# Kernel tuning notes

Measured on AMD Instinct MI355X. Metric: run time of the kernel, lower is better.

Reference implementation:

```python
import jax, jax.numpy as jnp
import numpy as np

N, E, NG = 4096, 8192, 256
AF, BF, H, L = 9, 4, 128, 3
LN_EPS = 1e-5


def _layernorm(x, g, b):
    mu = jnp.mean(x, axis=-1, keepdims=True)
    var = jnp.var(x, axis=-1, keepdims=True)
    return (x - mu) * jax.lax.rsqrt(var + LN_EPS) * g + b


def setup_inputs() -> dict:
    key = jax.random.key(0)
    ks = jax.random.split(key, 20)
    x = jax.random.normal(ks[0], (N, AF), dtype=jnp.float32)
    edge_index = jax.random.randint(ks[1], (2, E), 0, N, dtype=jnp.int64)
    edge_attr = jax.random.normal(ks[2], (E, BF), dtype=jnp.float32)
    batch = jnp.sort(jax.random.randint(ks[3], (N,), 0, NG, dtype=jnp.int64))
    s = lambda f: 1.0 / np.sqrt(f)
    return {
        "x": x, "edge_index": edge_index, "edge_attr": edge_attr, "batch": batch,
        "atom_w": jax.random.normal(ks[4], (AF, H), jnp.float32) * s(AF),
        "atom_b": jnp.zeros((H,), jnp.float32),
        # per-layer edge-network params, stacked over L layers
        "e1_w": jax.random.normal(ks[5], (L, BF, H), jnp.float32) * s(BF),
        "e1_b": jnp.zeros((L, H), jnp.float32),
        "e2_w": jax.random.normal(ks[6], (L, H, H * H), jnp.float32) * s(H),
        "e2_b": jnp.zeros((L, H * H), jnp.float32),
        "root_w": jax.random.normal(ks[7], (L, H, H), jnp.float32) * s(H),
        "conv_b": jnp.zeros((L, H), jnp.float32),
        "ln_g": jnp.ones((L, H), jnp.float32),
        "ln_b": jnp.zeros((L, H), jnp.float32),
        "head_w1": jax.random.normal(ks[8], (H, H // 2), jnp.float32) * s(H),
        "head_b1": jnp.zeros((H // 2,), jnp.float32),
        "head_w2": jax.random.normal(ks[9], (H // 2, 1), jnp.float32) * s(H // 2),
        "head_b2": jnp.zeros((1,), jnp.float32),
    }


def reference(x, edge_index, edge_attr, batch, atom_w, atom_b, e1_w, e1_b,
              e2_w, e2_b, root_w, conv_b, ln_g, ln_b, head_w1, head_b1,
              head_w2, head_b2):
    src, dst = edge_index[0], edge_index[1]
    h = jax.nn.relu(x @ atom_w + atom_b)  # [N, H]
    # in-degree for mean aggregation (empty -> 0 via clamp on denominator)
    deg = jax.ops.segment_sum(jnp.ones((E,), h.dtype), dst, num_segments=N)
    denom = jnp.maximum(deg, 1.0)[:, None]
    for l in range(L):
        # edge network: bond features -> per-edge HxH weight matrix
        eh = jax.nn.gelu(edge_attr @ e1_w[l] + e1_b[l], approximate=False)
        w = (eh @ e2_w[l] + e2_b[l]).reshape(E, H, H)  # [E, H, H]
        # gather source node features, per-edge matvec, scatter-mean to dst
        msg = jnp.einsum('ei,eio->eo', h[src], w)  # [E, H]
        agg = jax.ops.segment_sum(msg, dst, num_segments=N) / denom
        h_new = jax.nn.relu(agg + h @ root_w[l] + conv_b[l])
        h = _layernorm(h + h_new, ln_g[l], ln_b[l])
        # dropout: eval mode (identity)
    # global mean pool over graphs
    cnt = jnp.maximum(jax.ops.segment_sum(jnp.ones((N,), h.dtype), batch, num_segments=NG), 1.0)
    mol = jax.ops.segment_sum(h, batch, num_segments=NG) / cnt[:, None]
    hid = jax.nn.gelu(mol @ head_w1 + head_b1, approximate=False)
    logits = (hid @ head_w2 + head_b2).squeeze(-1)  # [NG]
    return logits
```

## Files before the change

kernel.cpp:

```cpp
#include <hip/hip_runtime.h>
#include <hip/hip_bf16.h>

#define N_NODES 4096
#define N_EDGES 8192
#define NGRAPH  256
#define AFEAT   9
#define BFEAT   4
#define H       128
#define NL      3
#define KS      129
#define SPLITS  8
#define SLICE_SH    16384
#define SLICE_BYTES 32768
#define HALF_BYTES  16384

typedef short short8 __attribute__((ext_vector_type(8)));
typedef short short4v __attribute__((ext_vector_type(4)));
typedef float f32x4 __attribute__((ext_vector_type(4)));

__device__ __forceinline__ short f2b(float f){
    union { float f; unsigned u; } c; c.f = f;
    unsigned r = c.u + 0x7FFFu + ((c.u >> 16) & 1u);
    return (short)(r >> 16);
}
__device__ __forceinline__ float b2f(short b){
    union { unsigned u; float f; } c;
    c.u = ((unsigned)(unsigned short)b) << 16;
    return c.f;
}
__device__ __forceinline__ float gelu_exact(float x){
    return 0.5f * x * (1.0f + erff(x * 0.70710678118654752440f));
}
__device__ __forceinline__ void async_copy16(const void* g, void* l){
    typedef __attribute__((address_space(1))) const char AS1C;
    typedef __attribute__((address_space(3))) char AS3;
    __builtin_amdgcn_global_load_lds((AS1C*)g, (AS3*)l, 16, 0, 0);
}

__global__ void k_prep_b(const float* __restrict__ e2w, const float* __restrict__ e2b,
                         short* __restrict__ bt){
    __shared__ float ts[H][33];
    int b  = blockIdx.x;
    int o0 = (b & 3) * 32;
    int k  = (b >> 2) % KS;
    int l  = (b >> 2) / KS;
    const float* src = (k < H) ? (e2w + ((size_t)l * H + k) * (H * H))
                               : (e2b + (size_t)l * (H * H));
    for (int idx = threadIdx.x; idx < H * 32; idx += 256){
        int i = idx >> 5, op = idx & 31;
        ts[i][op] = src[i * H + o0 + op];
    }
    __syncthreads();
    short* dst = bt + (size_t)(l * KS + k) * SLICE_SH;
    for (int idx = threadIdx.x; idx < 32 * H; idx += 256){
        int j    = idx & 7;
        int quad = (idx >> 3) & 3;
        int op   = (idx >> 5) & 31;
        int ic   = idx >> 10;
        int i    = ic * 32 + quad * 8 + j;
        int o    = o0 + op;
        dst[((((o >> 4) * 4 + ic) * 64) + quad * 16 + (o & 15)) * 8 + j] = f2b(ts[i][op]);
    }
}

__global__ void k_atom(const float* __restrict__ x, const float* __restrict__ aw,
                       const float* __restrict__ ab, float* __restrict__ h,
                       short* __restrict__ hb){
    __shared__ float xs[AFEAT];
    int n = blockIdx.x, o = threadIdx.x;
    if (o < AFEAT) xs[o] = x[n * AFEAT + o];
    __syncthreads();
    float a = ab[o];
    #pragma unroll
    for (int f = 0; f < AFEAT; ++f) a += xs[f] * aw[f * H + o];
    a = fmaxf(a, 0.0f);
    h[(size_t)n * H + o]  = a;
    hb[(size_t)n * H + o] = f2b(a);
}

__global__ void k_deg(const int* __restrict__ ei, int* __restrict__ ideg){
    int e = blockIdx.x * 256 + threadIdx.x;
    if (e < N_EDGES) atomicAdd(&ideg[ei[N_EDGES + e]], 1);
}

__global__ void k_scan(const int* __restrict__ ideg, int* __restrict__ row_ptr,
                       int* __restrict__ cursor){
    __shared__ int part[256];
    int t = threadIdx.x;
    int base = t * 16;
    int loc[16]; int s = 0;
    #pragma unroll
    for (int i = 0; i < 16; ++i){ loc[i] = s; s += ideg[base + i]; }
    part[t] = s;
    __syncthreads();
    if (t == 0){
        int run = 0;
        for (int i = 0; i < 256; ++i){ int v = part[i]; part[i] = run; run += v; }
        row_ptr[N_NODES] = run;
    }
    __syncthreads();
    int off = part[t];
    #pragma unroll
    for (int i = 0; i < 16; ++i){
        row_ptr[base + i] = off + loc[i];
        cursor[base + i]  = off + loc[i];
    }
}

__global__ void k_fill(const int* __restrict__ ei, int* __restrict__ cursor,
                       int* __restrict__ eidx){
    int e = blockIdx.x * 256 + threadIdx.x;
    if (e < N_EDGES){
        int d = ei[N_EDGES + e];
        int pos = atomicAdd(&cursor[d], 1);
        eidx[pos] = e;
    }
}

__global__ void k_edge_mlp(const float* __restrict__ ea, const float* __restrict__ w1,
                           const float* __restrict__ b1, short* __restrict__ ehT){
    __shared__ float as[BFEAT];
    int e = blockIdx.x, o = threadIdx.x;
    if (o < BFEAT) as[o] = ea[e * BFEAT + o];
    __syncthreads();
    #pragma unroll
    for (int l = 0; l < NL; ++l){
        float v = b1[l * H + o];
        #pragma unroll
        for (int f = 0; f < BFEAT; ++f) v += as[f] * w1[(l * BFEAT + f) * H + o];
        v = gelu_exact(v);
        ehT[((size_t)l * KS + o) * N_EDGES + e] = f2b(v);
        if (o == 0) ehT[((size_t)l * KS + H) * N_EDGES + e] = f2b(1.0f);
    }
}

__global__ __launch_bounds__(256, 2)
void k_msg_gemm(const short* __restrict__ bt, const short* __restrict__ ehT,
                const short* __restrict__ hb, const int* __restrict__ ei,
                float* __restrict__ parts, int l){
    __shared__ __align__(16) char smem[2 * HALF_BYTES + 17 * H * 2];
    short* ehs = (short*)(smem + 2 * HALF_BYTES);

    const int tid  = threadIdx.x;
    const int lane = tid & 63, w = tid >> 6;
    const int col  = lane & 15, quad = lane >> 4;
    const int wrow = w >> 1, wcol = w & 1;

    const int split = blockIdx.x & 7;
    const int oh    = (blockIdx.x >> 3) & 1;
    const int tile  = blockIdx.x >> 4;
    const int kbeg  = (KS * split) >> 3;
    const int kend  = (KS * (split + 1)) >> 3;
    const int kcnt  = kend - kbeg;
    const int ebase = tile * 128;

    for (int idx = tid; idx < kcnt * 128; idx += 256){
        int kk = idx >> 7, e = idx & 127;
        ehs[idx] = ehT[((size_t)(l * KS + kbeg + kk)) * N_EDGES + ebase + e];
    }

    short8 gf[4][4];
    #pragma unroll
    for (int m = 0; m < 4; ++m){
        int e = ebase + wrow * 64 + m * 16 + col;
        int s = ei[e];
        const char* gb = (const char*)hb + ((size_t)s * H + quad * 8) * 2;
        #pragma unroll
        for (int ic = 0; ic < 4; ++ic)
            gf[m][ic] = *(const short8*)(gb + ic * 64);
    }

    float acc[4][2][4];
    #pragma unroll
    for (int m = 0; m < 4; ++m)
        #pragma unroll
        for (int ot = 0; ot < 2; ++ot)
            #pragma unroll
            for (int r = 0; r < 4; ++r) acc[m][ot][r] = 0.0f;

    const char* bsrc = (const char*)bt + (size_t)(l * KS + kbeg) * SLICE_BYTES
                     + oh * HALF_BYTES;

    #pragma unroll
    for (int i = 0; i < 4; ++i){
        int c = w * 4 + i;
        async_copy16(bsrc + c * 1024 + lane * 16, smem + c * 1024 + lane * 16);
    }
    __syncthreads();

    for (int kk = 0; kk < kcnt; ++kk){
        __builtin_amdgcn_s_barrier();
        if (kk + 1 < kcnt){
            const char* g = bsrc + (size_t)(kk + 1) * SLICE_BYTES;
            char* d = smem + ((kk + 1) & 1) * HALF_BYTES;
            #pragma unroll
            for (int i = 0; i < 4; ++i){
                int c = w * 4 + i;
                async_copy16(g + c * 1024 + lane * 16, d + c * 1024 + lane * 16);
            }
            asm volatile("s_waitcnt vmcnt(4)" ::: "memory");
        } else {
            asm volatile("s_waitcnt vmcnt(0)" ::: "memory");
        }
        __builtin_amdgcn_s_barrier();

        const char* Bl = smem + (kk & 1) * HALF_BYTES;

        short4v ev[4];
        #pragma unroll
        for (int m = 0; m < 4; ++m)
            ev[m] = *(const short4v*)(ehs + kk * 128 + wrow * 64 + m * 16 + quad * 4);

        __builtin_amdgcn_s_setprio(1);
        #pragma unroll
        for (int ot = 0; ot < 2; ++ot){
            int tl = wcol * 2 + ot;
            short8 bf[4];
            #pragma unroll
            for (int ic = 0; ic < 4; ++ic)
                bf[ic] = *(const short8*)(Bl + (tl * 4 + ic) * 1024 + lane * 16);
            #pragma unroll
            for (int m = 0; m < 4; ++m){
                f32x4 U = {0.0f, 0.0f, 0.0f, 0.0f};
                #pragma unroll
                for (int ic = 0; ic < 4; ++ic)
                    U = __builtin_amdgcn_mfma_f32_16x16x32_bf16(gf[m][ic], bf[ic], U, 0, 0, 0);
                #pragma unroll
                for (int r = 0; r < 4; ++r)
                    acc[m][ot][r] += b2f(ev[m][r]) * U[r];
            }
        }
        __builtin_amdgcn_s_setprio(0);
    }

    float* pb = parts + (size_t)split * N_EDGES * H + (size_t)(ebase + wrow * 64) * H
              + oh * 64 + wcol * 32;
    #pragma unroll
    for (int m = 0; m < 4; ++m)
        #pragma unroll
        for (int r = 0; r < 4; ++r){
            float* row = pb + (m * 16 + quad * 4 + r) * H;
            #pragma unroll
            for (int ot = 0; ot < 2; ++ot)
                row[ot * 16 + col] = acc[m][ot][r];
        }
}

__global__ void k_node(const float* __restrict__ parts, const int* __restrict__ eidx,
                       const int* __restrict__ row_ptr,
                       const float* __restrict__ rw, const float* __restrict__ cb,
                       const float* __restrict__ lg, const float* __restrict__ lb,
                       float* __restrict__ h, short* __restrict__ hb, int l){
    __shared__ float hs[H];
    __shared__ float rsum[2], rsq[2];
    int n = blockIdx.x, o = threadIdx.x;
    float hv = h[(size_t)n * H + o];
    hs[o] = hv;
    int p0 = row_ptr[n], p1 = row_ptr[n + 1];
    float a = 0.0f;
    for (int p = p0; p < p1; ++p){
        const float* pr = parts + (size_t)eidx[p] * H + o;
        #pragma unroll
        for (int s = 0; s < SPLITS; ++s) a += pr[(size_t)s * N_EDGES * H];
    }
    int d = p1 - p0;
    a *= 1.0f / (float)(d > 0 ? d : 1);
    __syncthreads();
    float root = cb[l * H + o];
    const float* W = rw + (size_t)l * H * H;
    #pragma unroll 8
    for (int i = 0; i < H; ++i) root += hs[i] * W[i * H + o];
    float hn = fmaxf(a + root, 0.0f);
    float v  = hv + hn;
    float s = v, q = v * v;
    #pragma unroll
    for (int off = 32; off > 0; off >>= 1){
        s += __shfl_down(s, off, 64);
        q += __shfl_down(q, off, 64);
    }
    if ((o & 63) == 0){ rsum[o >> 6] = s; rsq[o >> 6] = q; }
    __syncthreads();
    float S = rsum[0] + rsum[1], Q = rsq[0] + rsq[1];
    float mean = S * (1.0f / H);
    float var  = Q * (1.0f / H) - mean * mean;
    float out  = (v - mean) * rsqrtf(var + 1e-5f) * lg[l * H + o] + lb[l * H + o];
    h[(size_t)n * H + o]  = out;
    hb[(size_t)n * H + o] = f2b(out);
}

__global__ void k_pool(const float* __restrict__ h, const int* __restrict__ batch,
                       float* __restrict__ molsum, float* __restrict__ cnt){
    int idx = blockIdx.x * 256 + threadIdx.x;
    int n = idx >> 7, o = idx & 127;
    int b = batch[n];
    atomicAdd(&molsum[b * H + o], h[idx]);
    if (o == 0) atomicAdd(&cnt[b], 1.0f);
}

__global__ void k_head(const float* __restrict__ molsum, const float* __restrict__ cnt,
                       const float* __restrict__ w1, const float* __restrict__ b1,
                       const float* __restrict__ w2, const float* __restrict__ b2,
                       float* __restrict__ out){
    __shared__ float mol[H];
    int g = blockIdx.x, t = threadIdx.x;
    float c = fmaxf(cnt[g], 1.0f);
    mol[t]      = molsum[g * H + t] / c;
    mol[t + 64] = molsum[g * H + t + 64] / c;
    __syncthreads();
    float a = b1[t];
    #pragma unroll 8
    for (int i = 0; i < H; ++i) a += mol[i] * w1[i * 64 + t];
    float hid = gelu_exact(a);
    float p = hid * w2[t];
    #pragma unroll
    for (int off = 32; off > 0; off >>= 1) p += __shfl_down(p, off, 64);
    if (t == 0) out[g] = p + b2[0];
}

extern "C" void kernel_launch(void* const* d_in, const int* in_sizes, int n_in,
                              void* d_out, int out_size, void* d_ws, size_t ws_size,
                              hipStream_t stream){
    (void)in_sizes; (void)n_in; (void)out_size; (void)ws_size;
    const float* x     = (const float*)d_in[0];
    const int*   ei    = (const int*)  d_in[1];
    const float* ea    = (const float*)d_in[2];
    const int*   batch = (const int*)  d_in[3];
    const float* aw    = (const float*)d_in[4];
    const float* ab    = (const float*)d_in[5];
    const float* e1w   = (const float*)d_in[6];
    const float* e1b   = (const float*)d_in[7];
    const float* e2w   = (const float*)d_in[8];
    const float* e2b   = (const float*)d_in[9];
    const float* rw    = (const float*)d_in[10];
    const float* cb    = (const float*)d_in[11];
    const float* lg    = (const float*)d_in[12];
    const float* lb    = (const float*)d_in[13];
    const float* hw1   = (const float*)d_in[14];
    const float* hb1   = (const float*)d_in[15];
    const float* hw2   = (const float*)d_in[16];
    const float* hb2   = (const float*)d_in[17];
    float* out = (float*)d_out;

    char* p = (char*)d_ws;
    auto carve = [&](size_t bytes){ char* r = p; p += (bytes + 255) & ~(size_t)255; return r; };
    short* bt     = (short*)carve((size_t)NL * KS * SLICE_SH * 2);
    float* h      = (float*)carve((size_t)N_NODES * H * 4);
    short* hbuf   = (short*)carve((size_t)N_NODES * H * 2);
    short* ehT    = (short*)carve((size_t)NL * KS * N_EDGES * 2);
    float* parts  = (float*)carve((size_t)SPLITS * N_EDGES * H * 4);
    int*   ideg   = (int*)  carve((size_t)N_NODES * 4);
    int*   row_ptr= (int*)  carve((size_t)(N_NODES + 1) * 4);
    int*   cursor = (int*)  carve((size_t)N_NODES * 4);
    int*   eidx   = (int*)  carve((size_t)N_EDGES * 4);
    float* molsum = (float*)carve((size_t)NGRAPH * H * 4);
    float* cnt    = (float*)carve((size_t)NGRAPH * 4);

    hipMemsetAsync(ideg, 0, (size_t)N_NODES * 4, stream);
    hipMemsetAsync(molsum, 0, (size_t)NGRAPH * H * 4, stream);
    hipMemsetAsync(cnt, 0, (size_t)NGRAPH * 4, stream);

    k_prep_b<<<NL * KS * 4, 256, 0, stream>>>(e2w, e2b, bt);
    k_atom<<<N_NODES, H, 0, stream>>>(x, aw, ab, h, hbuf);
    k_deg<<<N_EDGES / 256, 256, 0, stream>>>(ei, ideg);
    k_scan<<<1, 256, 0, stream>>>(ideg, row_ptr, cursor);
    k_fill<<<N_EDGES / 256, 256, 0, stream>>>(ei, cursor, eidx);
    k_edge_mlp<<<N_EDGES, H, 0, stream>>>(ea, e1w, e1b, ehT);

    for (int l = 0; l < NL; ++l){
        k_msg_gemm<<<64 * 2 * SPLITS, 256, 0, stream>>>(bt, ehT, hbuf, ei, parts, l);
        k_node<<<N_NODES, H, 0, stream>>>(parts, eidx, row_ptr, rw, cb, lg, lb, h, hbuf, l);
    }
    k_pool<<<N_NODES * H / 256, 256, 0, stream>>>(h, batch, molsum, cnt);
    k_head<<<NGRAPH, 64, 0, stream>>>(molsum, cnt, hw1, hb1, hw2, hb2, out);
}
```

Baseline: 331.4 us.

## Give each wave private double-buffered weight slices and halve the K-split count

The message GEMM now tiles 64 edges per block, and each of the four waves owns 32 output columns. Each wave streams its own 8 KB weight slice into a private double-buffered LDS region, so the two block-wide barriers per K step go away and only a per-wave lgkmcnt/vmcnt wait remains. The K split drops from 8 to 4, which halves the partial-sum buffer that k_node must read and reduce. In exchange, every weight slice is fetched once per 64 edges instead of once per 128, doubling weight traffic from L2. Gathered source features are also loaded redundantly by all four waves, and the grid shrinks to 512 blocks.

```diff
diff --git a/kernel.cpp b/kernel.cpp
--- a/kernel.cpp
+++ b/kernel.cpp
@@ -9,10 +9,11 @@
 #define H       128
 #define NL      3
 #define KS      129
-#define SPLITS  8
+#define SPLITS  4
+#define TILE_E  64
 #define SLICE_SH    16384
 #define SLICE_BYTES 32768
-#define HALF_BYTES  16384
+#define WREG_BYTES  8192
 
 typedef short short8 __attribute__((ext_vector_type(8)));
 typedef short short4v __attribute__((ext_vector_type(4)));
@@ -138,31 +139,29 @@
 void k_msg_gemm(const short* __restrict__ bt, const short* __restrict__ ehT,
                 const short* __restrict__ hb, const int* __restrict__ ei,
                 float* __restrict__ parts, int l){
-    __shared__ __align__(16) char smem[2 * HALF_BYTES + 17 * H * 2];
-    short* ehs = (short*)(smem + 2 * HALF_BYTES);
+    __shared__ __align__(16) char smem[2 * 4 * WREG_BYTES + 33 * TILE_E * 2];
+    short* ehs = (short*)(smem + 2 * 4 * WREG_BYTES);
 
     const int tid  = threadIdx.x;
     const int lane = tid & 63, w = tid >> 6;
     const int col  = lane & 15, quad = lane >> 4;
-    const int wrow = w >> 1, wcol = w & 1;
-
-    const int split = blockIdx.x & 7;
-    const int oh    = (blockIdx.x >> 3) & 1;
-    const int tile  = blockIdx.x >> 4;
-    const int kbeg  = (KS * split) >> 3;
-    const int kend  = (KS * (split + 1)) >> 3;
+
+    const int split = blockIdx.x & 3;
+    const int tile  = blockIdx.x >> 2;
+    const int kbeg  = (KS * split) >> 2;
+    const int kend  = (KS * (split + 1)) >> 2;
     const int kcnt  = kend - kbeg;
-    const int ebase = tile * 128;
-
-    for (int idx = tid; idx < kcnt * 128; idx += 256){
-        int kk = idx >> 7, e = idx & 127;
+    const int ebase = tile * TILE_E;
+
+    for (int idx = tid; idx < kcnt * TILE_E; idx += 256){
+        int kk = idx >> 6, e = idx & 63;
         ehs[idx] = ehT[((size_t)(l * KS + kbeg + kk)) * N_EDGES + ebase + e];
     }
 
     short8 gf[4][4];
     #pragma unroll
     for (int m = 0; m < 4; ++m){
-        int e = ebase + wrow * 64 + m * 16 + col;
+        int e = ebase + m * 16 + col;
         int s = ei[e];
         const char* gb = (const char*)hb + ((size_t)s * H + quad * 8) * 2;
         #pragma unroll
@@ -179,46 +178,41 @@
             for (int r = 0; r < 4; ++r) acc[m][ot][r] = 0.0f;
 
     const char* bsrc = (const char*)bt + (size_t)(l * KS + kbeg) * SLICE_BYTES
-                     + oh * HALF_BYTES;
-
-    #pragma unroll
-    for (int i = 0; i < 4; ++i){
-        int c = w * 4 + i;
-        async_copy16(bsrc + c * 1024 + lane * 16, smem + c * 1024 + lane * 16);
-    }
+                     + w * WREG_BYTES;
+    char* lws = smem + w * WREG_BYTES;
+
+    #pragma unroll
+    for (int i = 0; i < 8; ++i)
+        async_copy16(bsrc + i * 1024 + lane * 16, lws + i * 1024 + lane * 16);
+
     __syncthreads();
 
     for (int kk = 0; kk < kcnt; ++kk){
-        __builtin_amdgcn_s_barrier();
         if (kk + 1 < kcnt){
             const char* g = bsrc + (size_t)(kk + 1) * SLICE_BYTES;
-            char* d = smem + ((kk + 1) & 1) * HALF_BYTES;
-            #pragma unroll
-            for (int i = 0; i < 4; ++i){
-                int c = w * 4 + i;
-                async_copy16(g + c * 1024 + lane * 16, d + c * 1024 + lane * 16);
-            }
-            asm volatile("s_waitcnt vmcnt(4)" ::: "memory");
+            char* d = lws + ((kk + 1) & 1) * (4 * WREG_BYTES);
+            asm volatile("s_waitcnt lgkmcnt(0)" ::: "memory");
+            #pragma unroll
+            for (int i = 0; i < 8; ++i)
+                async_copy16(g + i * 1024 + lane * 16, d + i * 1024 + lane * 16);
+            asm volatile("s_waitcnt vmcnt(8)" ::: "memory");
         } else {
             asm volatile("s_waitcnt vmcnt(0)" ::: "memory");
         }
-        __builtin_amdgcn_s_barrier();
-
-        const char* Bl = smem + (kk & 1) * HALF_BYTES;
+        const char* Bl = lws + (kk & 1) * (4 * WREG_BYTES);
 
         short4v ev[4];
         #pragma unroll
         for (int m = 0; m < 4; ++m)
-            ev[m] = *(const short4v*)(ehs + kk * 128 + wrow * 64 + m * 16 + quad * 4);
+            ev[m] = *(const short4v*)(ehs + kk * TILE_E + m * 16 + quad * 4);
 
         __builtin_amdgcn_s_setprio(1);
         #pragma unroll
         for (int ot = 0; ot < 2; ++ot){
-            int tl = wcol * 2 + ot;
             short8 bf[4];
             #pragma unroll
             for (int ic = 0; ic < 4; ++ic)
-                bf[ic] = *(const short8*)(Bl + (tl * 4 + ic) * 1024 + lane * 16);
+                bf[ic] = *(const short8*)(Bl + (ot * 4 + ic) * 1024 + lane * 16);
             #pragma unroll
             for (int m = 0; m < 4; ++m){
                 f32x4 U = {0.0f, 0.0f, 0.0f, 0.0f};
@@ -233,8 +227,7 @@
         __builtin_amdgcn_s_setprio(0);
     }
 
-    float* pb = parts + (size_t)split * N_EDGES * H + (size_t)(ebase + wrow * 64) * H
-              + oh * 64 + wcol * 32;
+    float* pb = parts + (size_t)split * N_EDGES * H + (size_t)ebase * H + w * 32;
     #pragma unroll
     for (int m = 0; m < 4; ++m)
         #pragma unroll
@@ -367,7 +360,7 @@
     k_edge_mlp<<<N_EDGES, H, 0, stream>>>(ea, e1w, e1b, ehT);
 
     for (int l = 0; l < NL; ++l){
-        k_msg_gemm<<<64 * 2 * SPLITS, 256, 0, stream>>>(bt, ehT, hbuf, ei, parts, l);
+        k_msg_gemm<<<(N_EDGES / TILE_E) * SPLITS, 256, 0, stream>>>(bt, ehT, hbuf, ei, parts, l);
         k_node<<<N_NODES, H, 0, stream>>>(parts, eidx, row_ptr, rw, cb, lg, lb, h, hbuf, l);
     }
     k_pool<<<N_NODES * H / 256, 256, 0, stream>>>(h, batch, molsum, cnt);
```

New measurement: 320.1 us. 3.4% less time.
